# Kernel optimization log

Measured on AMD Instinct MI355X. Metric: run time of the kernel, lower is better.

## Reference

```python
import jax, jax.numpy as jnp
import numpy as np

B, S, D, H, DK, F, L, FEAT, T = 32, 256, 512, 8, 64, 2048, 6, 9, 100


def _pos_emb(seq_len, d):
    # 'transformers from scratch' style sinusoidal embedding
    pos = jnp.arange(seq_len, dtype=jnp.float32)[:, None]
    dim = jnp.arange(d, dtype=jnp.float32)[None, :]
    phase = pos / jnp.power(1e4, dim / d)
    return jnp.where(jnp.arange(d)[None, :] % 2 == 0, jnp.sin(phase), jnp.cos(phase))


def _ln(x, g, b, eps=1e-5):
    m = jnp.mean(x, -1, keepdims=True)
    v = jnp.mean((x - m) ** 2, -1, keepdims=True)
    return (x - m) * jax.lax.rsqrt(v + eps) * g + b


def _mha(q_in, k_in, v_in, wq, bq, wk, bk, wv, bv, wo, bo):
    # wq/wk/wv: [H, D, DK]; batched equivalent of per-head Linear projections
    q = jnp.einsum('bsd,hdk->bhsk', q_in, wq) + bq[:, None, :]
    k = jnp.einsum('bsd,hdk->bhsk', k_in, wk) + bk[:, None, :]
    v = jnp.einsum('bsd,hdk->bhsk', v_in, wv) + bv[:, None, :]
    scale = jnp.sqrt(jnp.asarray(q.shape[-1], jnp.float32))
    att = jax.nn.softmax(jnp.einsum('bhqk,bhsk->bhqs', q, k) / scale, axis=-1)
    o = jnp.einsum('bhqs,bhsv->bhqv', att, v)  # [B,H,S,DK]
    o = o.transpose(0, 2, 1, 3).reshape(q_in.shape[0], q_in.shape[1], -1)  # concat heads
    return o @ wo + bo


def setup_inputs() -> dict:
    key = jax.random.key(0)
    ks = iter(jax.random.split(key, 64))
    rn = lambda *sh: 0.02 * jax.random.normal(next(ks), sh, jnp.float32)
    d = {
        'tgt': jax.random.uniform(next(ks), (B, S, FEAT), jnp.float32),
        'memory': jax.random.normal(next(ks), (B, S, D), jnp.float32),
        'time': jax.random.randint(next(ks), (B, S), 0, T),
        'gender': jax.random.randint(next(ks), (B, 1), 0, 2),
        'race': jax.random.randint(next(ks), (B, 1), 0, 3),
        'mask': jax.random.uniform(next(ks), (B, S, FEAT), jnp.float32),
        'w_f2h': rn(FEAT, D), 'b_f2h': jnp.zeros((D,)),
        'emb_time': rn(T, D), 'emb_gender': rn(2, D), 'emb_race': rn(3, D),
        'wq1': rn(L, H, D, DK), 'bq1': jnp.zeros((L, H, DK)),
        'wk1': rn(L, H, D, DK), 'bk1': jnp.zeros((L, H, DK)),
        'wv1': rn(L, H, D, DK), 'bv1': jnp.zeros((L, H, DK)),
        'wo1': rn(L, H * DK, D), 'bo1': jnp.zeros((L, D)),
        'g1': jnp.ones((L, D)), 'be1': jnp.zeros((L, D)),
        'wq2': rn(L, H, D, DK), 'bq2': jnp.zeros((L, H, DK)),
        'wk2': rn(L, H, D, DK), 'bk2': jnp.zeros((L, H, DK)),
        'wv2': rn(L, H, D, DK), 'bv2': jnp.zeros((L, H, DK)),
        'wo2': rn(L, H * DK, D), 'bo2': jnp.zeros((L, D)),
        'g2': jnp.ones((L, D)), 'be2': jnp.zeros((L, D)),
        'w1f': rn(L, D, F), 'b1f': jnp.zeros((L, F)),
        'w2f': rn(L, F, D), 'b2f': jnp.zeros((L, D)),
        'gf': jnp.ones((L, D)), 'bff': jnp.zeros((L, D)),
        'w_out': rn(D, FEAT), 'b_out': jnp.zeros((FEAT,)),
        'w_m': rn(D, FEAT), 'b_m': jnp.zeros((FEAT,)),
    }
    return d


def reference(tgt, memory, time, gender, race, mask,
              w_f2h, b_f2h, emb_time, emb_gender, emb_race,
              wq1, bq1, wk1, bk1, wv1, bv1, wo1, bo1, g1, be1,
              wq2, bq2, wk2, bk2, wv2, bv2, wo2, bo2, g2, be2,
              w1f, b1f, w2f, b2f, gf, bff,
              w_out, b_out, w_m, b_m):
    # attentioned_mask=False, mask provided -> tgt = tgt * mask
    x = (tgt * mask) @ w_f2h + b_f2h  # feature2hidden
    x = x + _pos_emb(x.shape[1], x.shape[2])
    x = x + emb_time[time] + emb_gender[gender] + emb_race[race]  # [B,S,D] += [B,1,D]
    for l in range(L):
        # self-attention residual block (dropout is identity in eval)
        x = _ln(x + _mha(x, x, x, wq1[l], bq1[l], wk1[l], bk1[l], wv1[l], bv1[l], wo1[l], bo1[l]), g1[l], be1[l])
        # 'cross' block: q,k from memory, v from tgt; residual on tgt (tensors[-1])
        x = _ln(x + _mha(memory, memory, x, wq2[l], bq2[l], wk2[l], bk2[l], wv2[l], bv2[l], wo2[l], bo2[l]), g2[l], be2[l])
        # feed forward
        x = _ln(x + jax.nn.relu(x @ w1f[l] + b1f[l]) @ w2f[l] + b2f[l], gf[l], bff[l])
    output = jax.nn.sigmoid(x @ w_out + b_out)
    mask_out = jax.nn.sigmoid(x @ w_m + b_m)  # attentioned_mask=False -> linear_m(tgt)
    return output, time, mask_out
```

## Files before the change

kernel.cpp:

```cpp
#include <hip/hip_runtime.h>
#include <hip/hip_bf16.h>
#include <math.h>

constexpr int Bn   = 32;
constexpr int Sn   = 256;
constexpr int Dn   = 512;
constexpr int Hn   = 8;
constexpr int DKn  = 64;
constexpr int Fn   = 2048;
constexpr int Ln   = 6;
constexpr int FEATn= 9;
constexpr int BSn  = Bn * Sn;

typedef __hip_bfloat16 bf16;
typedef __attribute__((ext_vector_type(8))) short short8;
typedef __attribute__((ext_vector_type(4))) short short4v;
typedef __attribute__((ext_vector_type(4))) float f32x4;

#define GLOAD_LDS16(gp, lp)                                                   \
    __builtin_amdgcn_global_load_lds(                                         \
        (const __attribute__((address_space(1))) void*)(gp),                  \
        (__attribute__((address_space(3))) void*)(lp), 16, 0, 0)

#define BARRIER do {                                                          \
    __builtin_amdgcn_sched_barrier(0);                                        \
    asm volatile("" ::: "memory");                                            \
    __builtin_amdgcn_s_barrier();                                             \
    asm volatile("" ::: "memory");                                            \
    __builtin_amdgcn_sched_barrier(0);                                        \
} while (0)

#define VMCNT0 do {                                                           \
    asm volatile("s_waitcnt vmcnt(0)" ::: "memory");                          \
    __builtin_amdgcn_sched_barrier(0);                                        \
} while (0)

__device__ __forceinline__ short f2bs(float f) {
    __hip_bfloat16 h = __float2bfloat16(f);
    return *reinterpret_cast<short*>(&h);
}
__device__ __forceinline__ float bs2f(short s) {
    unsigned u = ((unsigned)(unsigned short)s) << 16;
    return *reinterpret_cast<float*>(&u);
}

__global__ __launch_bounds__(256)
void k_embed(const float* __restrict__ tgt, const float* __restrict__ mask,
             const float* __restrict__ w_f2h, const float* __restrict__ b_f2h,
             const int* __restrict__ timei, const int* __restrict__ gender,
             const int* __restrict__ race,
             const float* __restrict__ emb_t, const float* __restrict__ emb_g,
             const float* __restrict__ emb_r, bf16* __restrict__ x)
{
    int idx = blockIdx.x * 256 + threadIdx.x;
    int d  = idx & (Dn - 1);
    int bs = idx >> 9;
    int b  = bs / Sn;
    int s  = bs & (Sn - 1);
    const float* tg = tgt  + (size_t)bs * FEATn;
    const float* mk = mask + (size_t)bs * FEATn;
    float acc = b_f2h[d];
    #pragma unroll
    for (int f = 0; f < FEATn; ++f) acc += tg[f] * mk[f] * w_f2h[f * Dn + d];
    float phase = (float)s * expf(-((float)d / (float)Dn) * 9.210340372f);
    acc += (d & 1) ? cosf(phase) : sinf(phase);
    acc += emb_t[(size_t)timei[bs] * Dn + d];
    acc += emb_g[(size_t)gender[b] * Dn + d];
    acc += emb_r[(size_t)race[b]   * Dn + d];
    x[idx] = __float2bfloat16(acc);
}

__global__ __launch_bounds__(256)
void k_cvt(const float* __restrict__ in, bf16* __restrict__ out)
{
    int i = blockIdx.x * 256 + threadIdx.x;
    out[i] = __float2bfloat16(in[i]);
}

__global__ __launch_bounds__(256)
void k_tcvt6(const float* __restrict__ i0, bf16* __restrict__ o0,
             const float* __restrict__ i1, bf16* __restrict__ o1,
             const float* __restrict__ i2, bf16* __restrict__ o2,
             const float* __restrict__ i3, bf16* __restrict__ o3,
             const float* __restrict__ i4, bf16* __restrict__ o4,
             const float* __restrict__ i5, bf16* __restrict__ o5,
             int R, int C, int ZB)
{
    __shared__ float ts[32][33];
    const int sel = blockIdx.z / ZB, zi = blockIdx.z % ZB;
    const float* in  = sel == 0 ? i0 : sel == 1 ? i1 : sel == 2 ? i2
                     : sel == 3 ? i3 : sel == 4 ? i4 : i5;
    bf16*        out = sel == 0 ? o0 : sel == 1 ? o1 : sel == 2 ? o2
                     : sel == 3 ? o3 : sel == 4 ? o4 : o5;
    const int t  = threadIdx.x;
    const int tx = t & 31, ty = t >> 5;
    const int r0 = blockIdx.y * 32, c0 = blockIdx.x * 32;
    const size_t zo = (size_t)zi * R * C;
    #pragma unroll
    for (int i = 0; i < 4; ++i)
        ts[ty + 8 * i][tx] = in[zo + (size_t)(r0 + ty + 8 * i) * C + c0 + tx];
    __syncthreads();
    #pragma unroll
    for (int i = 0; i < 4; ++i)
        out[zo + (size_t)(c0 + ty + 8 * i) * R + r0 + tx] =
            __float2bfloat16(ts[tx][ty + 8 * i]);
}

__global__ __launch_bounds__(256)
void k_prep_final(const float* __restrict__ w_out, const float* __restrict__ b_out,
                  const float* __restrict__ w_m, const float* __restrict__ b_m,
                  bf16* __restrict__ Wcat, float* __restrict__ bcat)
{
    int idx = blockIdx.x * 256 + threadIdx.x;
    int n = idx >> 9, k = idx & 511;
    float v = 0.f;
    if (n < FEATn)          v = w_out[(size_t)k * FEATn + n];
    else if (n < 2 * FEATn) v = w_m[(size_t)k * FEATn + (n - FEATn)];
    Wcat[idx] = __float2bfloat16(v);
    if (idx < 32) {
        float bv = idx < FEATn ? b_out[idx]
                 : (idx < 2 * FEATn ? b_m[idx - FEATn] : 0.f);
        bcat[idx] = bv;
    }
}

template<int BM, int BN, bool RELU, bool RESID, bool TRANSV = false>
__global__ __launch_bounds__(256)
void k_gemm_bf(const bf16* __restrict__ A0, const bf16* __restrict__ A1,
               const bf16* __restrict__ A2,
               const bf16* __restrict__ W0, const bf16* __restrict__ W1,
               const bf16* __restrict__ W2,
               const float* __restrict__ bi0, const float* __restrict__ bi1,
               const float* __restrict__ bi2,
               const bf16* __restrict__ R,
               bf16* __restrict__ C0, bf16* __restrict__ C1, bf16* __restrict__ C2,
               int M, int N, int K, int MTt, int NTt, int ZN, int stat)
{
    constexpr int WTM = BM / 2, WTN = BN / 2;
    constexpr int MT  = WTM / 16, NT = WTN / 16;
    constexpr int NCA = BM / 64;
    constexpr int NCB = BN / 64;
    constexpr int CSTR   = BN + 8;
    constexpr int PASSES = BM / 64;

    const int id = blockIdx.x;
    const int c  = id & 7, j = id >> 3;
    int mt, nt, z;
    if (stat == 0) {
        const int inner = NTt * ZN;
        const int ml = j / inner, r = j - ml * inner;
        mt = c * (MTt >> 3) + ml;
        nt = r % NTt;
        z  = r / NTt;
    } else {
        const int inner = MTt * ZN;
        const int nl = j / inner, r = j - nl * inner;
        nt = c * (NTt >> 3) + nl;
        mt = r % MTt;
        z  = r / MTt;
    }
    const int m0 = mt * BM, n0 = nt * BN;

    const short* A   = (const short*)(z == 0 ? A0 : (z == 1 ? A1 : A2));
    const short* W   = (const short*)(z == 0 ? W0 : (z == 1 ? W1 : W2));
    const float* bia = (z == 0 ? bi0 : (z == 1 ? bi1 : bi2));
    bf16*        C   = (z == 0 ? C0 : (z == 1 ? C1 : C2));

    __shared__ __align__(16) short As[BM * 32];
    __shared__ __align__(16) short Bs[BN * 32];
    __shared__ __align__(16) short Cs[64 * CSTR];

    const int t    = threadIdx.x;
    const int w    = t >> 6, lane = t & 63;
    const int l16  = lane & 15, quad = lane >> 4;
    const int wm   = (w & 1) * WTM, wn = (w >> 1) * WTN;

    const short* Agp[NCA];
    const short* Bgp[NCB];
    #pragma unroll
    for (int i = 0; i < NCA; ++i) {
        const int cc = w * BM + i * 64 + lane;
        Agp[i] = A + (size_t)(m0 + (cc >> 2)) * K + (cc & 3) * 8;
    }
    #pragma unroll
    for (int i = 0; i < NCB; ++i) {
        const int cc = w * BN + i * 64 + lane;
        Bgp[i] = W + (size_t)(n0 + (cc >> 2)) * K + (cc & 3) * 8;
    }

    f32x4 acc[MT][NT] = {};
    const bool tv = TRANSV && (z == 2);

    for (int k0 = 0; k0 < K; k0 += 32) {
        #pragma unroll
        for (int i = 0; i < NCA; ++i) {
            GLOAD_LDS16(Agp[i], As + (w * BM + i * 64) * 8);
            Agp[i] += 32;
        }
        #pragma unroll
        for (int i = 0; i < NCB; ++i) {
            GLOAD_LDS16(Bgp[i], Bs + (w * BN + i * 64) * 8);
            Bgp[i] += 32;
        }
        __syncthreads();

        short8 af[MT], bf[NT];
        #pragma unroll
        for (int mi = 0; mi < MT; ++mi)
            af[mi] = *(const short8*)(As + (wm + mi * 16 + l16) * 32 + quad * 8);
        #pragma unroll
        for (int ni = 0; ni < NT; ++ni)
            bf[ni] = *(const short8*)(Bs + (wn + ni * 16 + l16) * 32 + quad * 8);
        if (tv) {
            #pragma unroll
            for (int mi = 0; mi < MT; ++mi)
                #pragma unroll
                for (int ni = 0; ni < NT; ++ni)
                    acc[mi][ni] = __builtin_amdgcn_mfma_f32_16x16x32_bf16(
                        bf[ni], af[mi], acc[mi][ni], 0, 0, 0);
        } else {
            #pragma unroll
            for (int mi = 0; mi < MT; ++mi)
                #pragma unroll
                for (int ni = 0; ni < NT; ++ni)
                    acc[mi][ni] = __builtin_amdgcn_mfma_f32_16x16x32_bf16(
                        af[mi], bf[ni], acc[mi][ni], 0, 0, 0);
        }
        __syncthreads();
    }

    if (tv) {
        constexpr int CPR = BM / 8;
        #pragma unroll
        for (int p = 0; p < PASSES; ++p) {
            if (PASSES == 1 || wn == p * 64) {
                #pragma unroll
                for (int ni = 0; ni < NT; ++ni) {
                    #pragma unroll
                    for (int r = 0; r < 4; ++r) {
                        const int lrow = wn - p * 64 + ni * 16 + quad * 4 + r;
                        const float bb = bia[n0 + p * 64 + lrow];
                        #pragma unroll
                        for (int mi = 0; mi < MT; ++mi)
                            Cs[lrow * CSTR + wm + mi * 16 + l16] =
                                f2bs(acc[mi][ni][r] + bb);
                    }
                }
            }
            __syncthreads();
            #pragma unroll
            for (int cc = 0; cc < 64 * CPR; cc += 256) {
                const int row = (cc + t) / CPR, colc = (cc + t) % CPR;
                short8 cv = *(const short8*)(Cs + row * CSTR + colc * 8);
                *(short8*)((short*)C + (size_t)(n0 + p * 64 + row) * M
                                      + m0 + colc * 8) = cv;
            }
            __syncthreads();
        }
    } else {
        constexpr int CPR = BN / 8;
        #pragma unroll
        for (int p = 0; p < PASSES; ++p) {
            if (PASSES == 1 || wm == p * 64) {
                #pragma unroll
                for (int ni = 0; ni < NT; ++ni) {
                    const float bb = bia[n0 + wn + ni * 16 + l16];
                    #pragma unroll
                    for (int mi = 0; mi < MT; ++mi) {
                        const int lrow0 = wm - p * 64 + mi * 16 + quad * 4;
                        #pragma unroll
                        for (int r = 0; r < 4; ++r) {
                            float v = acc[mi][ni][r] + bb;
                            if (RELU) v = fmaxf(v, 0.f);
                            Cs[(lrow0 + r) * CSTR + wn + ni * 16 + l16] = f2bs(v);
                        }
                    }
                }
            }
            __syncthreads();
            #pragma unroll
            for (int cc = 0; cc < 64 * CPR; cc += 256) {
                const int row = (cc + t) / CPR, colc = (cc + t) % CPR;
                const size_t goff = (size_t)(m0 + p * 64 + row) * N + n0 + colc * 8;
                short8 cv = *(const short8*)(Cs + row * CSTR + colc * 8);
                if (RESID) {
                    short8 rv = *(const short8*)((const short*)R + goff);
                    short8 ov;
                    #pragma unroll
                    for (int i = 0; i < 8; ++i)
                        ov[i] = f2bs(bs2f(cv[i]) + bs2f(rv[i]));
                    *(short8*)((short*)C + goff) = ov;
                } else {
                    *(short8*)((short*)C + goff) = cv;
                }
            }
            __syncthreads();
        }
    }
}

template<int RH, int CH, class STG, class FIN>
__device__ __forceinline__ void gemm8_phase(short* sm, int buf, int baseA,
                                            int baseB, f32x4 (&acc)[8][4],
                                            STG stg, FIN fin)
{
    short8 paf[2][4];
    short8 pbf[2][2];
    #pragma unroll
    for (int i = 0; i < 4; ++i) {
        const int a0 = buf + baseA + RH * 4096 + i * 1024;
        paf[0][i] = *(const short8*)(sm + a0);
        paf[1][i] = *(const short8*)(sm + (a0 ^ 32));
    }
    #pragma unroll
    for (int j = 0; j < 2; ++j) {
        const int b0 = buf + baseB + CH * 2048 + j * 1024;
        pbf[0][j] = *(const short8*)(sm + b0);
        pbf[1][j] = *(const short8*)(sm + (b0 ^ 32));
    }
    stg();
    BARRIER;
    __builtin_amdgcn_s_setprio(1);
    #pragma unroll
    for (int i = 0; i < 4; ++i)
        #pragma unroll
        for (int j = 0; j < 2; ++j) {
            acc[RH * 4 + i][CH * 2 + j] = __builtin_amdgcn_mfma_f32_16x16x32_bf16(
                paf[0][i], pbf[0][j], acc[RH * 4 + i][CH * 2 + j], 0, 0, 0);
            acc[RH * 4 + i][CH * 2 + j] = __builtin_amdgcn_mfma_f32_16x16x32_bf16(
                paf[1][i], pbf[1][j], acc[RH * 4 + i][CH * 2 + j], 0, 0, 0);
        }
    __builtin_amdgcn_s_setprio(0);
    fin();
    BARRIER;
}

template<bool RELU>
__global__ __launch_bounds__(512, 2)
void k_gemm8ph(const bf16* __restrict__ Ain, const bf16* __restrict__ Win,
               const float* __restrict__ bia, bf16* __restrict__ Cout,
               int M, int N, int K, int NTt)
{
    __shared__ __align__(16) short smem[65536];

    const int id  = blockIdx.x;
    const int cxd = id & 7, jj = id >> 3;
    const int mpx = (M >> 8) >> 3;
    const int ml  = jj / NTt, nl = jj % NTt;
    const int mt  = cxd * mpx + ml;
    const int m0  = mt * 256, n0 = nl * 256;

    const int t    = threadIdx.x;
    const int lane = t & 63, w = t >> 6;
    const int l16  = lane & 15, quad = lane >> 4;
    const int wr   = w >> 2, wc = w & 3;

    const short* A = (const short*)Ain;
    const short* W = (const short*)Win;

    const int rowL = t >> 3;
    const int cX   = (t & 7) ^ (rowL & 7);
    const short* pA00 = A + (size_t)(m0 +   0 +  0 + rowL) * K + cX * 8;
    const short* pA01 = A + (size_t)(m0 +   0 + 64 + rowL) * K + cX * 8;
    const short* pA10 = A + (size_t)(m0 + 128 +  0 + rowL) * K + cX * 8;
    const short* pA11 = A + (size_t)(m0 + 128 + 64 + rowL) * K + cX * 8;
    const short* pB00 = W + (size_t)(n0 +   0 +  0 + rowL) * K + cX * 8;
    const short* pB01 = W + (size_t)(n0 +   0 + 64 + rowL) * K + cX * 8;
    const short* pB10 = W + (size_t)(n0 + 128 +  0 + rowL) * K + cX * 8;
    const short* pB11 = W + (size_t)(n0 + 128 + 64 + rowL) * K + cX * 8;

    auto stageA = [&](int nb, int k2) {
        short* d = smem + nb * 16384 + t * 8;
        GLOAD_LDS16(pA00 + (size_t)k2 * 64, d);
        GLOAD_LDS16(pA01 + (size_t)k2 * 64, d + 4096);
        GLOAD_LDS16(pA10 + (size_t)k2 * 64, d + 8192);
        GLOAD_LDS16(pA11 + (size_t)k2 * 64, d + 12288);
    };
    auto stageB = [&](int nb, int k2) {
        short* d = smem + 32768 + nb * 16384 + t * 8;
        GLOAD_LDS16(pB00 + (size_t)k2 * 64, d);
        GLOAD_LDS16(pB01 + (size_t)k2 * 64, d + 4096);
        GLOAD_LDS16(pB10 + (size_t)k2 * 64, d + 8192);
        GLOAD_LDS16(pB11 + (size_t)k2 * 64, d + 12288);
    };

    const int axor  = (quad ^ (l16 & 7)) << 3;
    const int baseA = wr * 8192 + l16 * 64 + axor;
    const int baseB = 32768 + (wc >> 1) * 8192 + (wc & 1) * 4096
                    + l16 * 64 + axor;

    float bias_v[4];
    #pragma unroll
    for (int ni = 0; ni < 4; ++ni)
        bias_v[ni] = bia[n0 + wc * 64 + ni * 16 + l16];

    f32x4 acc[8][4] = {};

    stageA(0, 0);
    stageB(0, 0);
    VMCNT0;
    BARRIER;

    const int NKT = K >> 6;
    for (int kt = 0; kt < NKT; ++kt) {
        const int  buf = (kt & 1) << 14;
        const int  nb  = (kt + 1) & 1;
        const bool st  = (kt + 1) < NKT;
        gemm8_phase<0, 0>(smem, buf, baseA, baseB, acc,
                          [&] { if (st) stageA(nb, kt + 1); }, [&] {});
        gemm8_phase<0, 1>(smem, buf, baseA, baseB, acc,
                          [&] { if (st) stageB(nb, kt + 1); }, [&] {});
        gemm8_phase<1, 0>(smem, buf, baseA, baseB, acc, [&] {}, [&] {});
        gemm8_phase<1, 1>(smem, buf, baseA, baseB, acc, [&] {}, [&] { VMCNT0; });
    }

    #pragma unroll
    for (int p = 0; p < 2; ++p) {
        if (wr == p) {
            #pragma unroll
            for (int mi = 0; mi < 8; ++mi)
                #pragma unroll
                for (int ni = 0; ni < 4; ++ni)
                    #pragma unroll
                    for (int r = 0; r < 4; ++r) {
                        float v = acc[mi][ni][r] + bias_v[ni];
                        if (RELU) v = fmaxf(v, 0.f);
                        smem[(mi * 16 + quad * 4 + r) * 264
                             + wc * 64 + ni * 16 + l16] = f2bs(v);
                    }
        }
        BARRIER;
        #pragma unroll
        for (int i2 = 0; i2 < 8; ++i2) {
            const int idx = i2 * 512 + t;
            const int row = idx >> 5, chn = idx & 31;
            short8 cv = *(const short8*)(smem + row * 264 + chn * 8);
            *(short8*)((short*)Cout + (size_t)(m0 + p * 128 + row) * N
                                     + n0 + chn * 8) = cv;
        }
        BARRIER;
    }
}

__global__ __launch_bounds__(256)
void k_attn_mfma(const bf16* __restrict__ q, const bf16* __restrict__ k,
                 const bf16* __restrict__ vT, bf16* __restrict__ ocat)
{
    __shared__ __align__(16) short smem[33280];
    short* Vst = smem;
    short* Ks  = smem + 16384;
    short* Ps  = smem + 16384;
    short* Cs  = smem + 16384;

    const int t = threadIdx.x, w = t >> 6, lane = t & 63;
    const int l16 = lane & 15, quad = lane >> 4;
    const int qt = blockIdx.x >> 8;
    const int bh = blockIdx.x & 255;
    const int h  = bh & 7;
    const int b  = bh >> 3;
    const int q0 = qt * 64;

    const short* kg = (const short*)k  + (size_t)b * Sn * Dn + h * DKn;
    const short* qg = (const short*)q  + (size_t)b * Sn * Dn + h * DKn;
    const short* vg = (const short*)vT + (size_t)h * DKn * BSn + b * Sn;

    #pragma unroll
    for (int i = 0; i < 8; ++i) {
        const int c   = w * 512 + i * 64 + lane;
        const int key = c >> 3, cgk = (c & 7) ^ (key & 7);
        GLOAD_LDS16(kg + (size_t)key * Dn + cgk * 8, Ks + (w * 512 + i * 64) * 8);
        const int dv = c >> 5, cgv = (c & 31) ^ (dv & 7);
        GLOAD_LDS16(vg + (size_t)dv * BSn + cgv * 8, Vst + (w * 512 + i * 64) * 8);
    }

    const short* qp = qg + (size_t)(q0 + w * 16 + l16) * Dn + quad * 8;
    short8 bq0 = *(const short8*)(qp);
    short8 bq1 = *(const short8*)(qp + 32);
    __syncthreads();

    f32x4 accs[16];
    #pragma unroll
    for (int mi = 0; mi < 16; ++mi) accs[mi] = f32x4{0.f, 0.f, 0.f, 0.f};
    #pragma unroll
    for (int mi = 0; mi < 16; ++mi) {
        const int key = mi * 16 + l16;
        const int r0s = (quad     ^ (key & 7)) * 8;
        const int r1s = ((quad+4) ^ (key & 7)) * 8;
        short8 af0 = *(const short8*)(Ks + key * 64 + r0s);
        short8 af1 = *(const short8*)(Ks + key * 64 + r1s);
        accs[mi] = __builtin_amdgcn_mfma_f32_16x16x32_bf16(af0, bq0, accs[mi], 0, 0, 0);
        accs[mi] = __builtin_amdgcn_mfma_f32_16x16x32_bf16(af1, bq1, accs[mi], 0, 0, 0);
    }

    float mx = -1e30f;
    #pragma unroll
    for (int mi = 0; mi < 16; ++mi)
        #pragma unroll
        for (int r = 0; r < 4; ++r) mx = fmaxf(mx, accs[mi][r]);
    mx = fmaxf(mx, __shfl_xor(mx, 16));
    mx = fmaxf(mx, __shfl_xor(mx, 32));
    float sum = 0.f;
    #pragma unroll
    for (int mi = 0; mi < 16; ++mi)
        #pragma unroll
        for (int r = 0; r < 4; ++r) {
            float e = __expf((accs[mi][r] - mx) * 0.125f);
            accs[mi][r] = e;
            sum += e;
        }
    sum += __shfl_xor(sum, 16);
    sum += __shfl_xor(sum, 32);
    const float rs = 1.f / sum;

    __syncthreads();

    short* pr = Ps + (w * 16 + l16) * 264;
    #pragma unroll
    for (int mi = 0; mi < 16; ++mi) {
        short4v pk;
        pk.x = f2bs(accs[mi][0] * rs);
        pk.y = f2bs(accs[mi][1] * rs);
        pk.z = f2bs(accs[mi][2] * rs);
        pk.w = f2bs(accs[mi][3] * rs);
        *(short4v*)(pr + mi * 16 + quad * 4) = pk;
    }
    __syncthreads();

    f32x4 acco[4];
    #pragma unroll
    for (int nt = 0; nt < 4; ++nt) acco[nt] = f32x4{0.f, 0.f, 0.f, 0.f};
    #pragma unroll
    for (int k0 = 0; k0 < 8; ++k0) {
        short8 pa = *(const short8*)(pr + k0 * 32 + quad * 8);
        #pragma unroll
        for (int nt = 0; nt < 4; ++nt) {
            const int dv = nt * 16 + l16;
            const int sl = ((4 * k0 + quad) ^ (dv & 7)) * 8;
            short8 vb = *(const short8*)(Vst + dv * 256 + sl);
            acco[nt] = __builtin_amdgcn_mfma_f32_16x16x32_bf16(pa, vb, acco[nt], 0, 0, 0);
        }
    }
    __syncthreads();

    #pragma unroll
    for (int nt = 0; nt < 4; ++nt)
        #pragma unroll
        for (int r = 0; r < 4; ++r)
            Cs[(w * 16 + quad * 4 + r) * 72 + nt * 16 + l16] = f2bs(acco[nt][r]);
    __syncthreads();
    #pragma unroll
    for (int c = 0; c < 512; c += 256) {
        const int row = (c + t) >> 3, colc = (c + t) & 7;
        short8 cv = *(const short8*)(Cs + row * 72 + colc * 8);
        *(short8*)((short*)ocat + (size_t)(b * Sn + q0 + row) * Dn
                                 + h * DKn + colc * 8) = cv;
    }
}

__global__ __launch_bounds__(256)
void k_ln(const bf16* __restrict__ y, const float* __restrict__ g,
          const float* __restrict__ be, bf16* __restrict__ xo)
{
    const int t = threadIdx.x, w = t >> 6, lane = t & 63;
    const int row = blockIdx.x * 4 + w;
    const short* yr = (const short*)y + (size_t)row * Dn + lane * 8;
    short8 v8 = *(const short8*)yr;
    float f[8];
    float s1 = 0.f, s2 = 0.f;
    #pragma unroll
    for (int i = 0; i < 8; ++i) {
        f[i] = bs2f(v8[i]);
        s1 += f[i];
        s2 += f[i] * f[i];
    }
    #pragma unroll
    for (int off = 1; off < 64; off <<= 1) {
        s1 += __shfl_xor(s1, off);
        s2 += __shfl_xor(s2, off);
    }
    const float mean = s1 * (1.f / Dn);
    const float var  = s2 * (1.f / Dn) - mean * mean;
    const float isd  = rsqrtf(var + 1e-5f);
    const float4 g0 = *(const float4*)(g  + lane * 8);
    const float4 g1 = *(const float4*)(g  + lane * 8 + 4);
    const float4 b0 = *(const float4*)(be + lane * 8);
    const float4 b1 = *(const float4*)(be + lane * 8 + 4);
    const float gg[8] = {g0.x, g0.y, g0.z, g0.w, g1.x, g1.y, g1.z, g1.w};
    const float bb[8] = {b0.x, b0.y, b0.z, b0.w, b1.x, b1.y, b1.z, b1.w};
    short8 o8;
    #pragma unroll
    for (int i = 0; i < 8; ++i)
        o8[i] = f2bs((f[i] - mean) * isd * gg[i] + bb[i]);
    *(short8*)((short*)xo + (size_t)row * Dn + lane * 8) = o8;
}

__global__ __launch_bounds__(256)
void k_final2(const bf16* __restrict__ x, const bf16* __restrict__ Wcat,
              const float* __restrict__ bcat, const int* __restrict__ timei,
              float* __restrict__ out)
{
    const int t = threadIdx.x, w = t >> 6, lane = t & 63;
    const int l16 = lane & 15, quad = lane >> 4;
    const int r0 = blockIdx.x * 64 + w * 16;
    const short* xp = (const short*)x + (size_t)(r0 + l16) * Dn + quad * 8;
    const short* wp = (const short*)Wcat + (size_t)l16 * Dn + quad * 8;

    f32x4 acc[2] = {};
    #pragma unroll
    for (int kk = 0; kk < 16; ++kk) {
        short8 af = *(const short8*)(xp + kk * 32);
        short8 b0 = *(const short8*)(wp + kk * 32);
        short8 b1 = *(const short8*)(wp + 16 * Dn + kk * 32);
        acc[0] = __builtin_amdgcn_mfma_f32_16x16x32_bf16(af, b0, acc[0], 0, 0, 0);
        acc[1] = __builtin_amdgcn_mfma_f32_16x16x32_bf16(af, b1, acc[1], 0, 0, 0);
    }

    #pragma unroll
    for (int nt = 0; nt < 2; ++nt) {
        const int col = nt * 16 + l16;
        const float bb = bcat[col];
        #pragma unroll
        for (int r = 0; r < 4; ++r) {
            const int row = r0 + quad * 4 + r;
            float v = acc[nt][r] + bb;
            float sg = 1.f / (1.f + expf(-v));
            if (col < FEATn)
                out[(size_t)row * FEATn + col] = sg;
            else if (col < 2 * FEATn)
                out[(size_t)BSn * FEATn + BSn + (size_t)row * FEATn + (col - FEATn)] = sg;
        }
    }
    if (l16 == 0) {
        #pragma unroll
        for (int r = 0; r < 4; ++r) {
            const int row = r0 + quad * 4 + r;
            out[(size_t)BSn * FEATn + row] = (float)timei[row];
        }
    }
}

extern "C" void kernel_launch(void* const* d_in, const int* in_sizes, int n_in,
                              void* d_out, int out_size, void* d_ws, size_t ws_size,
                              hipStream_t stream)
{
    const float* tgt    = (const float*)d_in[0];
    const float* memory = (const float*)d_in[1];
    const int*   timei  = (const int*)  d_in[2];
    const int*   gender = (const int*)  d_in[3];
    const int*   race   = (const int*)  d_in[4];
    const float* maskp  = (const float*)d_in[5];
    const float* w_f2h  = (const float*)d_in[6];
    const float* b_f2h  = (const float*)d_in[7];
    const float* emb_t  = (const float*)d_in[8];
    const float* emb_g  = (const float*)d_in[9];
    const float* emb_r  = (const float*)d_in[10];
    const float* wq1 = (const float*)d_in[11]; const float* bq1 = (const float*)d_in[12];
    const float* wk1 = (const float*)d_in[13]; const float* bk1 = (const float*)d_in[14];
    const float* wv1 = (const float*)d_in[15]; const float* bv1 = (const float*)d_in[16];
    const float* wo1 = (const float*)d_in[17]; const float* bo1 = (const float*)d_in[18];
    const float* g1  = (const float*)d_in[19]; const float* be1 = (const float*)d_in[20];
    const float* wq2 = (const float*)d_in[21]; const float* bq2 = (const float*)d_in[22];
    const float* wk2 = (const float*)d_in[23]; const float* bk2 = (const float*)d_in[24];
    const float* wv2 = (const float*)d_in[25]; const float* bv2 = (const float*)d_in[26];
    const float* wo2 = (const float*)d_in[27]; const float* bo2 = (const float*)d_in[28];
    const float* g2  = (const float*)d_in[29]; const float* be2 = (const float*)d_in[30];
    const float* w1f = (const float*)d_in[31]; const float* b1f = (const float*)d_in[32];
    const float* w2f = (const float*)d_in[33]; const float* b2f = (const float*)d_in[34];
    const float* gfp = (const float*)d_in[35]; const float* bff = (const float*)d_in[36];
    const float* w_out = (const float*)d_in[37]; const float* b_out = (const float*)d_in[38];
    const float* w_m   = (const float*)d_in[39]; const float* b_m   = (const float*)d_in[40];
    float* out = (float*)d_out;

    constexpr size_t WH  = 1572864;
    constexpr size_t WF  = 6291456;
    constexpr size_t NA  = (size_t)BSn * Dn;
    bf16* wsb   = (bf16*)d_ws;
    bf16* wq1t  = wsb;
    bf16* wk1t  = wq1t + WH;
    bf16* wv1t  = wk1t + WH;
    bf16* wo1t  = wv1t + WH;
    bf16* wq2t  = wo1t + WH;
    bf16* wk2t  = wq2t + WH;
    bf16* wv2t  = wk2t + WH;
    bf16* wo2t  = wv2t + WH;
    bf16* w1ft  = wo2t + WH;
    bf16* w2ft  = w1ft + WF;
    bf16* memb  = w2ft + WF;
    bf16* x     = memb + NA;
    bf16* b1    = x  + NA;
    bf16* b2    = b1 + NA;
    bf16* b3    = b2 + NA;
    bf16* b4    = b3 + NA;
    bf16* h1    = b1;
    bf16* wcat  = b4 + NA;
    float* bcat = (float*)(wcat + 32 * Dn);

    dim3 blk(256);

    k_tcvt6<<<dim3( 2, 16, 288), blk, 0, stream>>>(
        wq1, wq1t, wk1, wk1t, wv1, wv1t, wq2, wq2t, wk2, wk2t, wv2, wv2t,
        512, 64, 48);
    k_tcvt6<<<dim3(16, 16, 12), blk, 0, stream>>>(
        wo1, wo1t, wo2, wo2t, wo1, wo1t, wo1, wo1t, wo1, wo1t, wo1, wo1t,
        512, 512, 6);
    k_tcvt6<<<dim3(64, 16, 6), blk, 0, stream>>>(
        w1f, w1ft, w1f, w1ft, w1f, w1ft, w1f, w1ft, w1f, w1ft, w1f, w1ft,
        512, 2048, 6);
    k_tcvt6<<<dim3(16, 64, 6), blk, 0, stream>>>(
        w2f, w2ft, w2f, w2ft, w2f, w2ft, w2f, w2ft, w2f, w2ft, w2f, w2ft,
        2048, 512, 6);
    k_cvt <<<dim3(NA / 256), blk, 0, stream>>>(memory, memb);
    k_prep_final<<<dim3(64), blk, 0, stream>>>(w_out, b_out, w_m, b_m, wcat, bcat);

    k_embed<<<dim3((BSn * Dn) / 256), blk, 0, stream>>>(
        tgt, maskp, w_f2h, b_f2h, timei, gender, race, emb_t, emb_g, emb_r, x);

    dim3 gP3(64 * 4 * 3);
    dim3 gP6(128 * 8);
    dim3 g8 (32 * 8);
    dim3 blk8(512);
    dim3 gA (Bn * Hn * 4);
    dim3 gL (BSn / 4);
    constexpr size_t WSL = 262144;
    constexpr size_t WFL = 1048576;

    for (int l = 0; l < Ln; ++l) {
        k_gemm_bf<128, 128, false, false, true><<<gP3, blk, 0, stream>>>(
            x, x, x,
            wq1t + l * WSL, wk1t + l * WSL, wv1t + l * WSL,
            bq1 + l * Dn, bk1 + l * Dn, bv1 + l * Dn,
            nullptr, b1, b2, b3, BSn, Dn, Dn, 64, 4, 3, 0);
        k_attn_mfma<<<gA, blk, 0, stream>>>(b1, b2, b3, b4);
        k_gemm_bf<64, 64, false, true><<<gP6, blk, 0, stream>>>(
            b4, b4, b4, wo1t + l * WSL, wo1t + l * WSL, wo1t + l * WSL,
            bo1 + l * Dn, bo1 + l * Dn, bo1 + l * Dn,
            x, x, x, x, BSn, Dn, Dn, 128, 8, 1, 0);
        k_ln<<<gL, blk, 0, stream>>>(x, g1 + l * Dn, be1 + l * Dn, x);
        k_gemm_bf<128, 128, false, false, true><<<gP3, blk, 0, stream>>>(
            memb, memb, x,
            wq2t + l * WSL, wk2t + l * WSL, wv2t + l * WSL,
            bq2 + l * Dn, bk2 + l * Dn, bv2 + l * Dn,
            nullptr, b1, b2, b3, BSn, Dn, Dn, 64, 4, 3, 0);
        k_attn_mfma<<<gA, blk, 0, stream>>>(b1, b2, b3, b4);
        k_gemm_bf<64, 64, false, true><<<gP6, blk, 0, stream>>>(
            b4, b4, b4, wo2t + l * WSL, wo2t + l * WSL, wo2t + l * WSL,
            bo2 + l * Dn, bo2 + l * Dn, bo2 + l * Dn,
            x, x, x, x, BSn, Dn, Dn, 128, 8, 1, 0);
        k_ln<<<gL, blk, 0, stream>>>(x, g2 + l * Dn, be2 + l * Dn, x);
        k_gemm8ph<true><<<g8, blk8, 0, stream>>>(
            x, w1ft + l * WFL, b1f + l * Fn, h1, BSn, Fn, Dn, 8);
        k_gemm_bf<64, 64, false, true><<<gP6, blk, 0, stream>>>(
            h1, h1, h1, w2ft + l * WFL, w2ft + l * WFL, w2ft + l * WFL,
            b2f + l * Dn, b2f + l * Dn, b2f + l * Dn,
            x, x, x, x, BSn, Dn, Fn, 128, 8, 1, 0);
        k_ln<<<gL, blk, 0, stream>>>(x, gfp + l * Dn, bff + l * Dn, x);
    }

    k_final2<<<dim3(BSn / 64), blk, 0, stream>>>(x, wcat, bcat, timei, out);
}
```

Measured before the change: 1.536 ms.

## Use 256x256 eight-wave phased GEMM kernel for fused QKV projections

```diff
diff --git a/kernel.cpp b/kernel.cpp
--- a/kernel.cpp
+++ b/kernel.cpp
@@ -32,6 +32,11 @@
 
 #define VMCNT0 do {                                                           \
     asm volatile("s_waitcnt vmcnt(0)" ::: "memory");                          \
+    __builtin_amdgcn_sched_barrier(0);                                        \
+} while (0)
+
+#define LGKM0 do {                                                            \
+    asm volatile("s_waitcnt lgkmcnt(0)" ::: "memory");                        \
     __builtin_amdgcn_sched_barrier(0);                                        \
 } while (0)
 
@@ -429,6 +434,7 @@
                              + wc * 64 + ni * 16 + l16] = f2bs(v);
                     }
         }
+        LGKM0;
         BARRIER;
         #pragma unroll
         for (int i2 = 0; i2 < 8; ++i2) {
@@ -438,7 +444,151 @@
             *(short8*)((short*)Cout + (size_t)(m0 + p * 128 + row) * N
                                      + n0 + chn * 8) = cv;
         }
+        LGKM0;
         BARRIER;
+    }
+}
+
+__global__ __launch_bounds__(512, 2)
+void k_qkv8ph(const bf16* __restrict__ Aqk, const bf16* __restrict__ Av,
+              const bf16* __restrict__ Wq, const bf16* __restrict__ Wk,
+              const bf16* __restrict__ Wv,
+              const float* __restrict__ bq, const float* __restrict__ bk,
+              const float* __restrict__ bv,
+              bf16* __restrict__ Cq, bf16* __restrict__ Ck,
+              bf16* __restrict__ Vt)
+{
+    __shared__ __align__(16) short smem[65536];
+
+    constexpr int K = Dn;
+    const int id  = blockIdx.x;
+    const int cxd = id & 7, jj = id >> 3;
+    const int ml  = jj / 6, nl = jj % 6;
+    const int mt  = cxd * 4 + ml;
+    const int m0  = mt * 256;
+    const int sel = nl >> 1;
+    const int n0l = (nl & 1) * 256;
+
+    const short* A = (const short*)(sel < 2 ? Aqk : Av);
+    const short* W = (const short*)(sel == 0 ? Wq : sel == 1 ? Wk : Wv);
+    const float* bia = sel == 0 ? bq : sel == 1 ? bk : bv;
+
+    const int t    = threadIdx.x;
+    const int lane = t & 63, w = t >> 6;
+    const int l16  = lane & 15, quad = lane >> 4;
+    const int wr   = w >> 2, wc = w & 3;
+
+    const int rowL = t >> 3;
+    const int cX   = (t & 7) ^ (rowL & 7);
+    const short* pA00 = A + (size_t)(m0 +   0 +  0 + rowL) * K + cX * 8;
+    const short* pA01 = A + (size_t)(m0 +   0 + 64 + rowL) * K + cX * 8;
+    const short* pA10 = A + (size_t)(m0 + 128 +  0 + rowL) * K + cX * 8;
+    const short* pA11 = A + (size_t)(m0 + 128 + 64 + rowL) * K + cX * 8;
+    const short* pB00 = W + (size_t)(n0l +   0 +  0 + rowL) * K + cX * 8;
+    const short* pB01 = W + (size_t)(n0l +   0 + 64 + rowL) * K + cX * 8;
+    const short* pB10 = W + (size_t)(n0l + 128 +  0 + rowL) * K + cX * 8;
+    const short* pB11 = W + (size_t)(n0l + 128 + 64 + rowL) * K + cX * 8;
+
+    auto stageA = [&](int nb, int k2) {
+        short* d = smem + nb * 16384 + t * 8;
+        GLOAD_LDS16(pA00 + (size_t)k2 * 64, d);
+        GLOAD_LDS16(pA01 + (size_t)k2 * 64, d + 4096);
+        GLOAD_LDS16(pA10 + (size_t)k2 * 64, d + 8192);
+        GLOAD_LDS16(pA11 + (size_t)k2 * 64, d + 12288);
+    };
+    auto stageB = [&](int nb, int k2) {
+        short* d = smem + 32768 + nb * 16384 + t * 8;
+        GLOAD_LDS16(pB00 + (size_t)k2 * 64, d);
+        GLOAD_LDS16(pB01 + (size_t)k2 * 64, d + 4096);
+        GLOAD_LDS16(pB10 + (size_t)k2 * 64, d + 8192);
+        GLOAD_LDS16(pB11 + (size_t)k2 * 64, d + 12288);
+    };
+
+    const int axor  = (quad ^ (l16 & 7)) << 3;
+    const int baseA = wr * 8192 + l16 * 64 + axor;
+    const int baseB = 32768 + (wc >> 1) * 8192 + (wc & 1) * 4096
+                    + l16 * 64 + axor;
+
+    float bias_v[4];
+    #pragma unroll
+    for (int ni = 0; ni < 4; ++ni)
+        bias_v[ni] = bia[n0l + wc * 64 + ni * 16 + l16];
+
+    f32x4 acc[8][4] = {};
+
+    stageA(0, 0);
+    stageB(0, 0);
+    VMCNT0;
+    BARRIER;
+
+    constexpr int NKT = K >> 6;
+    for (int kt = 0; kt < NKT; ++kt) {
+        const int  buf = (kt & 1) << 14;
+        const int  nb  = (kt + 1) & 1;
+        const bool st  = (kt + 1) < NKT;
+        gemm8_phase<0, 0>(smem, buf, baseA, baseB, acc,
+                          [&] { if (st) stageA(nb, kt + 1); }, [&] {});
+        gemm8_phase<0, 1>(smem, buf, baseA, baseB, acc,
+                          [&] { if (st) stageB(nb, kt + 1); }, [&] {});
+        gemm8_phase<1, 0>(smem, buf, baseA, baseB, acc, [&] {}, [&] {});
+        gemm8_phase<1, 1>(smem, buf, baseA, baseB, acc, [&] {}, [&] { VMCNT0; });
+    }
+
+    if (sel < 2) {
+        bf16* C = sel == 0 ? Cq : Ck;
+        #pragma unroll
+        for (int p = 0; p < 2; ++p) {
+            if (wr == p) {
+                #pragma unroll
+                for (int mi = 0; mi < 8; ++mi)
+                    #pragma unroll
+                    for (int ni = 0; ni < 4; ++ni)
+                        #pragma unroll
+                        for (int r = 0; r < 4; ++r)
+                            smem[(mi * 16 + quad * 4 + r) * 264
+                                 + wc * 64 + ni * 16 + l16] =
+                                f2bs(acc[mi][ni][r] + bias_v[ni]);
+            }
+            LGKM0;
+            BARRIER;
+            #pragma unroll
+            for (int i2 = 0; i2 < 8; ++i2) {
+                const int idx = i2 * 512 + t;
+                const int row = idx >> 5, chn = idx & 31;
+                short8 cv = *(const short8*)(smem + row * 264 + chn * 8);
+                *(short8*)((short*)C + (size_t)(m0 + p * 128 + row) * Dn
+                                     + n0l + chn * 8) = cv;
+            }
+            LGKM0;
+            BARRIER;
+        }
+    } else {
+        #pragma unroll
+        for (int p = 0; p < 4; ++p) {
+            if (wc == p) {
+                #pragma unroll
+                for (int mi = 0; mi < 8; ++mi)
+                    #pragma unroll
+                    for (int ni = 0; ni < 4; ++ni)
+                        #pragma unroll
+                        for (int r = 0; r < 4; ++r)
+                            smem[(ni * 16 + l16) * 264
+                                 + wr * 128 + mi * 16 + quad * 4 + r] =
+                                f2bs(acc[mi][ni][r] + bias_v[ni]);
+            }
+            LGKM0;
+            BARRIER;
+            #pragma unroll
+            for (int i2 = 0; i2 < 4; ++i2) {
+                const int idx = i2 * 512 + t;
+                const int row = idx >> 5, chn = idx & 31;
+                short8 cv = *(const short8*)(smem + row * 264 + chn * 8);
+                *(short8*)((short*)Vt + (size_t)(n0l + p * 64 + row) * BSn
+                                      + m0 + chn * 8) = cv;
+            }
+            LGKM0;
+            BARRIER;
+        }
     }
 }
 
@@ -715,7 +865,7 @@
     k_embed<<<dim3((BSn * Dn) / 256), blk, 0, stream>>>(
         tgt, maskp, w_f2h, b_f2h, timei, gender, race, emb_t, emb_g, emb_r, x);
 
-    dim3 gP3(64 * 4 * 3);
+    dim3 gQ (192);
     dim3 gP6(128 * 8);
     dim3 g8 (32 * 8);
     dim3 blk8(512);
@@ -725,22 +875,22 @@
     constexpr size_t WFL = 1048576;
 
     for (int l = 0; l < Ln; ++l) {
-        k_gemm_bf<128, 128, false, false, true><<<gP3, blk, 0, stream>>>(
-            x, x, x,
+        k_qkv8ph<<<gQ, blk8, 0, stream>>>(
+            x, x,
             wq1t + l * WSL, wk1t + l * WSL, wv1t + l * WSL,
             bq1 + l * Dn, bk1 + l * Dn, bv1 + l * Dn,
-            nullptr, b1, b2, b3, BSn, Dn, Dn, 64, 4, 3, 0);
+            b1, b2, b3);
         k_attn_mfma<<<gA, blk, 0, stream>>>(b1, b2, b3, b4);
         k_gemm_bf<64, 64, false, true><<<gP6, blk, 0, stream>>>(
             b4, b4, b4, wo1t + l * WSL, wo1t + l * WSL, wo1t + l * WSL,
             bo1 + l * Dn, bo1 + l * Dn, bo1 + l * Dn,
             x, x, x, x, BSn, Dn, Dn, 128, 8, 1, 0);
         k_ln<<<gL, blk, 0, stream>>>(x, g1 + l * Dn, be1 + l * Dn, x);
-        k_gemm_bf<128, 128, false, false, true><<<gP3, blk, 0, stream>>>(
-            memb, memb, x,
+        k_qkv8ph<<<gQ, blk8, 0, stream>>>(
+            memb, x,
             wq2t + l * WSL, wk2t + l * WSL, wv2t + l * WSL,
             bq2 + l * Dn, bk2 + l * Dn, bv2 + l * Dn,
-            nullptr, b1, b2, b3, BSn, Dn, Dn, 64, 4, 3, 0);
+            b1, b2, b3);
         k_attn_mfma<<<gA, blk, 0, stream>>>(b1, b2, b3, b4);
         k_gemm_bf<64, 64, false, true><<<gP6, blk, 0, stream>>>(
             b4, b4, b4, wo2t + l * WSL, wo2t + l * WSL, wo2t + l * WSL,
```

Measured after the change: 1.381 ms. 1.11x faster.
